# Kernel optimization log

Measured on AMD Instinct MI355X. Metric: run time of the kernel, lower is better.

Reference implementation:

```python
import jax, jax.numpy as jnp
import numpy as np

B, Q, DIM, HEADS, RPE_H, HGRID, WGRID, STRIDE = 2, 900, 256, 8, 512, 64, 64, 16
KV = HGRID * WGRID


def setup_inputs() -> dict:
    key = jax.random.key(0)
    ks = jax.random.split(key, 16)
    s = 0.02
    return {
        "hidden_states": jax.random.normal(ks[0], (B, Q, DIM), jnp.float32),
        "reference_points": jax.random.uniform(ks[1], (B, Q, 1, 4), jnp.float32),
        "key_value_states": jax.random.normal(ks[2], (B, KV, DIM), jnp.float32),
        "spatial_shapes": jnp.array([[HGRID, WGRID]], dtype=jnp.int64),
        "attention_mask": jax.random.randint(ks[3], (B, KV), 0, 2, jnp.int32),
        "mlp1_w1": jax.random.normal(ks[4], (RPE_H, 2), jnp.float32) * s,
        "mlp1_b1": jnp.zeros((RPE_H,), jnp.float32),
        "mlp1_w2": jax.random.normal(ks[5], (HEADS, RPE_H), jnp.float32) * s,
        "mlp2_w1": jax.random.normal(ks[6], (RPE_H, 2), jnp.float32) * s,
        "mlp2_b1": jnp.zeros((RPE_H,), jnp.float32),
        "mlp2_w2": jax.random.normal(ks[7], (HEADS, RPE_H), jnp.float32) * s,
        "q_w": jax.random.normal(ks[8], (DIM, DIM), jnp.float32) * s,
        "q_b": jnp.zeros((DIM,), jnp.float32),
        "k_w": jax.random.normal(ks[9], (DIM, DIM), jnp.float32) * s,
        "k_b": jnp.zeros((DIM,), jnp.float32),
        "v_w": jax.random.normal(ks[10], (DIM, DIM), jnp.float32) * s,
        "v_b": jnp.zeros((DIM,), jnp.float32),
        "o_w": jax.random.normal(ks[11], (DIM, DIM), jnp.float32) * s,
        "o_b": jnp.zeros((DIM,), jnp.float32),
    }


def _attn(hidden_states, reference_points, key_value_states, h, w, attention_mask,
          mlp1_w1, mlp1_b1, mlp1_w2, mlp2_w1, mlp2_b1, mlp2_w2,
          q_w, q_b, k_w, k_b, v_w, v_b, o_w, o_b):
    b, q_len, dim = hidden_states.shape
    nh = mlp1_w2.shape[0]
    hd = dim // nh
    scale = hd ** -0.5
    stride = STRIDE

    # boxes cxcywh -> x1y1x2y2, scaled to absolute pixel coords (reparam=False)
    c, sz = reference_points[..., :2], reference_points[..., 2:]
    ref = jnp.concatenate([c - sz / 2, c + sz / 2], axis=-1)  # (B,Q,1,4)
    mult = jnp.array([w * stride, h * stride, w * stride, h * stride], dtype=ref.dtype)
    ref = ref * mult

    pos_x = (jnp.arange(w, dtype=jnp.float32) + 0.5) * stride
    pos_y = (jnp.arange(h, dtype=jnp.float32) + 0.5) * stride
    dx = ref[..., 0::2] - pos_x[None, None, :, None]  # (B,Q,W,2)
    dy = ref[..., 1::2] - pos_y[None, None, :, None]  # (B,Q,H,2)

    # small MLPs: 2 -> rpe_hidden -> num_heads
    rpe_x = jax.nn.relu(dx @ mlp1_w1.T + mlp1_b1) @ mlp1_w2.T  # (B,Q,W,nh)
    rpe_y = jax.nn.relu(dy @ mlp2_w1.T + mlp2_b1) @ mlp2_w2.T  # (B,Q,H,nh)
    rpe = rpe_x[:, :, None, :, :] + rpe_y[:, :, :, None, :]    # (B,Q,H,W,nh)
    rpe = rpe.reshape(b, q_len, h * w, nh).transpose(0, 3, 1, 2)  # (B,nh,Q,K)

    queries = (hidden_states @ q_w.T + q_b).reshape(b, q_len, nh, hd).transpose(0, 2, 1, 3) * scale
    kv_len = key_value_states.shape[1]
    keys = (key_value_states @ k_w.T + k_b).reshape(b, kv_len, nh, hd).transpose(0, 2, 1, 3)
    values = (key_value_states @ v_w.T + v_b).reshape(b, kv_len, nh, hd).transpose(0, 2, 1, 3)

    scores = jnp.einsum('bhqd,bhkd->bhqk', queries, keys) + rpe
    scores = scores + attention_mask.astype(scores.dtype)[:, None, None] * (-100.0)
    probs = jax.nn.softmax(scores, axis=-1)
    ctx = jnp.einsum('bhqk,bhkd->bhqd', probs, values)
    ctx = ctx.transpose(0, 2, 1, 3).reshape(b, q_len, dim)
    return ctx @ o_w.T + o_b


def reference(hidden_states, reference_points, key_value_states, spatial_shapes, attention_mask,
              mlp1_w1, mlp1_b1, mlp1_w2, mlp2_w1, mlp2_b1, mlp2_w2,
              q_w, q_b, k_w, k_b, v_w, v_b, o_w, o_b):
    h = int(spatial_shapes[0, 0])
    w = int(spatial_shapes[0, 1])
    return _attn(hidden_states, reference_points, key_value_states, h, w, attention_mask,
                 mlp1_w1, mlp1_b1, mlp1_w2, mlp2_w1, mlp2_b1, mlp2_w2,
                 q_w, q_b, k_w, k_b, v_w, v_b, o_w, o_b)
```

## Files before the change

### kernel.cpp

```cpp
#include <hip/hip_runtime.h>
#include <math.h>

#define NB    2
#define NQ    900
#define NQP   960
#define NKV   4096
#define DIMM  256
#define NHEAD 8
#define HD    32
#define RPEH  512
#define GRID  64
#define SPLIT 4
#define KVSEG 1024
#define NT    16

typedef short short8 __attribute__((ext_vector_type(8)));
typedef float f32x4 __attribute__((ext_vector_type(4)));
typedef unsigned uint2v __attribute__((ext_vector_type(2)));
typedef unsigned short u16;
typedef unsigned short u16x4 __attribute__((ext_vector_type(4)));

__device__ inline u16 f2bf(float f) {
    unsigned u = __builtin_bit_cast(unsigned, f);
    u += 0x7fff + ((u >> 16) & 1);
    return (u16)(u >> 16);
}
__device__ inline unsigned packbf2(float a, float b) {
    unsigned ua = __builtin_bit_cast(unsigned, a);
    ua += 0x7fff + ((ua >> 16) & 1);
    unsigned ub = __builtin_bit_cast(unsigned, b);
    ub += 0x7fff + ((ub >> 16) & 1);
    return (ua >> 16) | (ub & 0xffff0000u);
}

#define HS4  115200
#define KV4  524288
#define W4   16384
__global__ __launch_bounds__(256) void conv_bf16(
    const float* __restrict__ hs, const float* __restrict__ kv,
    const float* __restrict__ qw, const float* __restrict__ kw,
    const float* __restrict__ vw,
    u16* __restrict__ hsbf, u16* __restrict__ kvbf,
    u16* __restrict__ qwbf, u16* __restrict__ kwbf, u16* __restrict__ vwbf)
{
    const int total = HS4 + KV4 + 3 * W4;
    for (int g = blockIdx.x * 256 + threadIdx.x; g < total; g += gridDim.x * 256) {
        const float* s; u16* d; int off;
        if (g < HS4)                       { s = hs; d = hsbf; off = g; }
        else if (g < HS4 + KV4)            { s = kv; d = kvbf; off = g - HS4; }
        else if (g < HS4 + KV4 + W4)       { s = qw; d = qwbf; off = g - HS4 - KV4; }
        else if (g < HS4 + KV4 + 2 * W4)   { s = kw; d = kwbf; off = g - HS4 - KV4 - W4; }
        else                               { s = vw; d = vwbf; off = g - HS4 - KV4 - 2 * W4; }
        f32x4 v = *(const f32x4*)(s + (size_t)off * 4);
        *(u16x4*)(d + (size_t)off * 4) =
            (u16x4){f2bf(v[0]), f2bf(v[1]), f2bf(v[2]), f2bf(v[3])};
    }
}

__global__ __launch_bounds__(256) void proj_mfma(
    const u16* __restrict__ A,
    const u16* __restrict__ W0, const float* __restrict__ B0,
    const u16* __restrict__ W1, const float* __restrict__ B1,
    u16* __restrict__ outRow, u16* __restrict__ outVt,
    int M, float scale)
{
    __shared__ u16 Abuf[2][4096];
    __shared__ u16 Bbuf[2][4096];

    const u16* W = W0; const float* bias = B0; bool vt = false;
    if (blockIdx.z == 1) { W = W1; bias = B1; vt = true; }

    const int t    = threadIdx.x;
    const int lane = t & 63;
    const int w    = t >> 6;
    const int wm   = w >> 1, wn = w & 1;
    const int m0   = blockIdx.x * 128;
    const int n0   = blockIdx.y * 128;

    const int r0 = t >> 2, c0 = t & 3;
    const int r1 = r0 + 64;
    const int s0 = r0 * 4 + (c0 ^ (r0 & 3));
    const int s1 = r1 * 4 + (c0 ^ (r1 & 3));
    const u16* Arow0 = A + (size_t)(m0 + r0) * DIMM + c0 * 8;
    const u16* Arow1 = A + (size_t)(m0 + r1) * DIMM + c0 * 8;
    const u16* Wrow0 = W + (size_t)(n0 + r0) * DIMM + c0 * 8;
    const u16* Wrow1 = W + (size_t)(n0 + r1) * DIMM + c0 * 8;

    const int fr = lane & 15, fkc = lane >> 4;
    int aslot[4], bslot[4];
    #pragma unroll
    for (int f = 0; f < 4; ++f) {
        int ar = wm * 64 + f * 16 + fr;
        int br = wn * 64 + f * 16 + fr;
        aslot[f] = ar * 4 + (fkc ^ (ar & 3));
        bslot[f] = br * 4 + (fkc ^ (br & 3));
    }
    float bv[4];
    #pragma unroll
    for (int f = 0; f < 4; ++f) bv[f] = bias[n0 + wn * 64 + f * 16 + fr];

    f32x4 acc[4][4] = {};

    {
        short8 a0 = *(const short8*)(Arow0);
        short8 a1 = *(const short8*)(Arow1);
        short8 b0 = *(const short8*)(Wrow0);
        short8 b1 = *(const short8*)(Wrow1);
        *(short8*)&Abuf[0][s0 * 8] = a0;
        *(short8*)&Abuf[0][s1 * 8] = a1;
        *(short8*)&Bbuf[0][s0 * 8] = b0;
        *(short8*)&Bbuf[0][s1 * 8] = b1;
    }
    __syncthreads();

    int cur = 0;
    for (int kt = 0; kt < 8; ++kt) {
        short8 na0, na1, nb0, nb1;
        if (kt < 7) {
            int ko = (kt + 1) * 32;
            na0 = *(const short8*)(Arow0 + ko);
            na1 = *(const short8*)(Arow1 + ko);
            nb0 = *(const short8*)(Wrow0 + ko);
            nb1 = *(const short8*)(Wrow1 + ko);
        }
        short8 af[4], bf[4];
        #pragma unroll
        for (int f = 0; f < 4; ++f) {
            af[f] = *(const short8*)&Abuf[cur][aslot[f] * 8];
            bf[f] = *(const short8*)&Bbuf[cur][bslot[f] * 8];
        }
        #pragma unroll
        for (int i = 0; i < 4; ++i)
            #pragma unroll
            for (int j = 0; j < 4; ++j)
                acc[i][j] = __builtin_amdgcn_mfma_f32_16x16x32_bf16(af[i], bf[j], acc[i][j], 0, 0, 0);
        if (kt < 7) {
            *(short8*)&Abuf[cur ^ 1][s0 * 8] = na0;
            *(short8*)&Abuf[cur ^ 1][s1 * 8] = na1;
            *(short8*)&Bbuf[cur ^ 1][s0 * 8] = nb0;
            *(short8*)&Bbuf[cur ^ 1][s1 * 8] = nb1;
        }
        __syncthreads();
        cur ^= 1;
    }

    #pragma unroll
    for (int i = 0; i < 4; ++i) {
        int mbase = m0 + wm * 64 + i * 16 + 4 * fkc;
        #pragma unroll
        for (int j = 0; j < 4; ++j) {
            int n = n0 + wn * 64 + j * 16 + fr;
            #pragma unroll
            for (int r = 0; r < 4; ++r) {
                int gm = mbase + r;
                if (gm < M) {
                    float v = (acc[i][j][r] + bv[j]) * scale;
                    if (!vt) {
                        outRow[(size_t)gm * DIMM + n] = f2bf(v);
                    } else {
                        int bb = gm >> 12, kvi = gm & 4095;
                        int hh = n >> 5, dd = n & 31;
                        outVt[(size_t)((bb * NHEAD + hh) * HD + dd) * NKV + kvi] = f2bf(v);
                    }
                }
            }
        }
    }
}

__global__ __launch_bounds__(256) void rpe_kernel(
    const float* __restrict__ ref_pts,
    const float* __restrict__ w1x, const float* __restrict__ b1x,
    const float* __restrict__ w2x,
    const float* __restrict__ w1y, const float* __restrict__ b1y,
    const float* __restrict__ w2y,
    float* __restrict__ rpex, float* __restrict__ rpey)
{
    __shared__ f32x4 wpk[RPEH];
    __shared__ float w2t[RPEH][NHEAD];

    const int t = threadIdx.x;
    const int m = blockIdx.x & 1;
    const int bq0 = (blockIdx.x >> 1) * 4;

    const float* w1 = m ? w1y : w1x;
    const float* b1 = m ? b1y : b1x;
    const float* w2 = m ? w2y : w2x;
    for (int r = t; r < RPEH; r += 256) {
        float a = w1[r * 2], b = w1[r * 2 + 1];
        wpk[r] = (f32x4){a, b, b1[r], a + b};
    }
    for (int i = t; i < RPEH * NHEAD; i += 256) {
        int h = i >> 9, r = i & 511;
        w2t[r][h] = w2[h * RPEH + r];
    }
    __syncthreads();

    const int lane = t & 63;
    const int w    = t >> 6;
    const int bq   = bq0 + w;
    const float p  = (lane + 0.5f) * 16.f;

    const float* q = ref_pts + (size_t)bq * 4;
    const float c = m ? q[1] : q[0];
    const float s = m ? q[3] : q[2];
    const float lo = (c - s * 0.5f) * 1024.f;
    const float hi = (c + s * 0.5f) * 1024.f;

    float acc[8] = {};
    #pragma unroll 4
    for (int r = 0; r < RPEH; ++r) {
        f32x4 W  = wpk[r];
        f32x4 u0 = *(const f32x4*)&w2t[r][0];
        f32x4 u1 = *(const f32x4*)&w2t[r][4];
        float al  = W[0] * lo + W[1] * hi + W[2];
        float hid = fmaxf(al - W[3] * p, 0.f);
        acc[0] += u0[0] * hid;
        acc[1] += u0[1] * hid;
        acc[2] += u0[2] * hid;
        acc[3] += u0[3] * hid;
        acc[4] += u1[0] * hid;
        acc[5] += u1[1] * hid;
        acc[6] += u1[2] * hid;
        acc[7] += u1[3] * hid;
    }

    float* outp = m ? rpey : rpex;
    size_t base = (size_t)bq * (NHEAD * GRID) + lane;
    #pragma unroll
    for (int h = 0; h < 8; ++h) outp[base + h * GRID] = acc[h];
}

__global__ __launch_bounds__(256) void attn_mfma(
    const u16* __restrict__ Qbf, const u16* __restrict__ Kbf,
    const u16* __restrict__ Vt,
    const float* __restrict__ RX, const float* __restrict__ RY,
    const int* __restrict__ mask,
    float* __restrict__ pctx, float2* __restrict__ pml)
{
    __shared__ short8 kbuf[2][4][64];
    __shared__ short8 vbuf[2][4][64];
    __shared__ unsigned pbuf[4][2][64][4];
    __shared__ float ry_s[16][68];
    __shared__ float mbuf[2][64];

    const int tid  = threadIdx.x;
    const int lane = tid & 63;
    const int w    = tid >> 6;
    const int q15  = lane & 15;
    const int g    = lane >> 4;
    const int qt = blockIdx.x, h = blockIdx.y;
    const int b  = blockIdx.z >> 2;
    const int sp = blockIdx.z & 3;
    const int q0 = qt * 64;
    const int wq = w * 16 + q15;
    const int gq = q0 + wq;
    const bool qok = gq < NQ;
    const int kv0g = sp * KVSEG;

    float rxr[16];
    {
        const float* rxrow = RX + (size_t)(b * NQ + (qok ? gq : 0)) * (NHEAD * GRID) + h * GRID;
        #pragma unroll
        for (int kt = 0; kt < 4; ++kt)
            #pragma unroll
            for (int r = 0; r < 4; ++r)
                rxr[kt * 4 + r] = qok ? rxrow[16 * kt + 4 * g + r] : 0.f;
    }
    for (int idx = tid; idx < 16 * 64; idx += 256) {
        int y = idx & 15, q = idx >> 4;
        int gq2 = q0 + q;
        ry_s[y][q] = (gq2 < NQ)
            ? RY[(size_t)(b * NQ + gq2) * (NHEAD * GRID) + h * GRID + sp * 16 + y] : 0.f;
    }

    short8 qf = *(const short8*)(Qbf + ((size_t)(b * NQ + gq)) * DIMM + h * HD + 8 * g);

    const int sr = tid >> 2, sc = tid & 3;
    const int vd = tid >> 3, vc = tid & 7;
    const size_t kbase = ((size_t)(b * NKV + kv0g + sr)) * DIMM + h * HD + 8 * sc;
    const size_t vbase = ((size_t)((b * NHEAD + h) * HD + vd)) * NKV + kv0g + 8 * vc;

    kbuf[0][sr >> 4][(sr & 15) + 16 * sc] = *(const short8*)(Kbf + kbase);
    vbuf[0][(vc >> 2) * 2 + (vd >> 4)][16 * (vc & 3) + (vd & 15)] = *(const short8*)(Vt + vbase);
    if (tid < 64) mbuf[0][tid] = -100.f * (float)mask[b * NKV + kv0g + tid];
    __syncthreads();

    f32x4 cacc0 = {0.f, 0.f, 0.f, 0.f};
    f32x4 cacc1 = {0.f, 0.f, 0.f, 0.f};
    float m_run = -1e30f, l_run = 0.f;
    int cur = 0;

    for (int t = 0; t < NT; ++t) {
        short8 rk = {}, rv = {};
        float rm = 0.f;
        if (t < NT - 1) {
            size_t kvn = (size_t)(t + 1) * 64;
            rk = *(const short8*)(Kbf + kbase + kvn * DIMM);
            rv = *(const short8*)(Vt + vbase + kvn);
            if (tid < 64) rm = -100.f * (float)mask[b * NKV + kv0g + kvn + tid];
        }

        f32x4 zero = {0.f, 0.f, 0.f, 0.f};
        f32x4 s[4];
        __builtin_amdgcn_s_setprio(1);
        #pragma unroll
        for (int kt = 0; kt < 4; ++kt)
            s[kt] = __builtin_amdgcn_mfma_f32_16x16x32_bf16(kbuf[cur][kt][lane], qf, zero, 0, 0, 0);
        __builtin_amdgcn_s_setprio(0);

        float ryb = ry_s[t][wq];
        #pragma unroll
        for (int kt = 0; kt < 4; ++kt) {
            #pragma unroll
            for (int r = 0; r < 4; ++r)
                s[kt][r] += rxr[kt * 4 + r] + ryb + mbuf[cur][16 * kt + 4 * g + r];
        }

        float mloc = s[0][0];
        #pragma unroll
        for (int kt = 0; kt < 4; ++kt)
            #pragma unroll
            for (int r = 0; r < 4; ++r) mloc = fmaxf(mloc, s[kt][r]);
        mloc = fmaxf(mloc, __shfl_xor(mloc, 16));
        mloc = fmaxf(mloc, __shfl_xor(mloc, 32));
        float mnew = fmaxf(m_run, mloc);
        float fsc  = __expf(m_run - mnew);
        float psum = 0.f;
        #pragma unroll
        for (int kt = 0; kt < 4; ++kt)
            #pragma unroll
            for (int r = 0; r < 4; ++r) {
                float pv = __expf(s[kt][r] - mnew);
                s[kt][r] = pv;
                psum += pv;
            }
        psum += __shfl_xor(psum, 16);
        psum += __shfl_xor(psum, 32);
        l_run = l_run * fsc + psum;
        m_run = mnew;
        cacc0 *= fsc;
        cacc1 *= fsc;

        #pragma unroll
        for (int kt = 0; kt < 4; ++kt) {
            unsigned d0 = packbf2(s[kt][0], s[kt][1]);
            unsigned d1 = packbf2(s[kt][2], s[kt][3]);
            int lt = 16 * ((2 * kt + (g >> 1)) & 3) + q15;
            uint2v* dst = (uint2v*)&pbuf[w][kt >> 1][lt][2 * (g & 1)];
            *dst = (uint2v){d0, d1};
        }

        __builtin_amdgcn_s_setprio(1);
        #pragma unroll
        for (int sk = 0; sk < 2; ++sk) {
            short8 pf = *(const short8*)&pbuf[w][sk][lane][0];
            cacc0 = __builtin_amdgcn_mfma_f32_16x16x32_bf16(vbuf[cur][sk * 2 + 0][lane], pf, cacc0, 0, 0, 0);
            cacc1 = __builtin_amdgcn_mfma_f32_16x16x32_bf16(vbuf[cur][sk * 2 + 1][lane], pf, cacc1, 0, 0, 0);
        }
        __builtin_amdgcn_s_setprio(0);

        if (t < NT - 1) {
            kbuf[cur ^ 1][sr >> 4][(sr & 15) + 16 * sc] = rk;
            vbuf[cur ^ 1][(vc >> 2) * 2 + (vd >> 4)][16 * (vc & 3) + (vd & 15)] = rv;
            if (tid < 64) mbuf[cur ^ 1][tid] = rm;
        }
        __syncthreads();
        cur ^= 1;
    }

    size_t prow = (size_t)(sp * NB + b) * NQP + gq;
    float* pc = pctx + prow * DIMM + h * HD;
    #pragma unroll
    for (int r = 0; r < 4; ++r) {
        pc[4 * g + r]      = cacc0[r];
        pc[16 + 4 * g + r] = cacc1[r];
    }
    if (g == 0) {
        float2 v; v.x = m_run; v.y = l_run;
        pml[prow * NHEAD + h] = v;
    }
}

__global__ __launch_bounds__(256) void attn_reduce(
    const float* __restrict__ pctx, const float2* __restrict__ pml,
    float* __restrict__ CTX)
{
    const int bq = blockIdx.x;
    const int b = bq / NQ, q = bq - b * NQ;
    const int c = threadIdx.x;
    const int h = c >> 5;

    float m[SPLIT], l[SPLIT];
    #pragma unroll
    for (int sp = 0; sp < SPLIT; ++sp) {
        float2 v = pml[((size_t)(sp * NB + b) * NQP + q) * NHEAD + h];
        m[sp] = v.x; l[sp] = v.y;
    }
    float ms = fmaxf(fmaxf(m[0], m[1]), fmaxf(m[2], m[3]));
    float L = 0.f, acc = 0.f;
    #pragma unroll
    for (int sp = 0; sp < SPLIT; ++sp) {
        float wgt = __expf(m[sp] - ms);
        L   += wgt * l[sp];
        acc += wgt * pctx[((size_t)(sp * NB + b) * NQP + q) * DIMM + c];
    }
    CTX[(size_t)bq * DIMM + c] = acc / L;
}

__global__ __launch_bounds__(256) void gemm_bias_f32(
    const float* __restrict__ A, const float* __restrict__ W,
    const float* __restrict__ bias, float* __restrict__ C,
    int M, int N, int K)
{
    __shared__ float As[32][33];
    __shared__ float Ws[32][33];
    const int t  = threadIdx.x;
    const int tr = t >> 4;
    const int tc = t & 15;
    const int brow = blockIdx.y * 32;
    const int bcol = blockIdx.x * 32;
    float acc00 = 0.f, acc01 = 0.f, acc10 = 0.f, acc11 = 0.f;

    for (int kt = 0; kt < K; kt += 32) {
        #pragma unroll
        for (int i = 0; i < 4; ++i) {
            int idx = t + i * 256;
            int r = idx >> 5, c = idx & 31;
            int gr = brow + r;
            As[r][c] = (gr < M) ? A[(size_t)gr * K + kt + c] : 0.f;
            Ws[r][c] = W[(size_t)(bcol + r) * K + kt + c];
        }
        __syncthreads();
        #pragma unroll 8
        for (int k = 0; k < 32; ++k) {
            float a0 = As[tr * 2][k], a1 = As[tr * 2 + 1][k];
            float w0 = Ws[tc * 2][k], w1 = Ws[tc * 2 + 1][k];
            acc00 += a0 * w0; acc01 += a0 * w1;
            acc10 += a1 * w0; acc11 += a1 * w1;
        }
        __syncthreads();
    }
    int gc0 = bcol + tc * 2, gc1 = gc0 + 1;
    int gr0 = brow + tr * 2, gr1 = gr0 + 1;
    if (gr0 < M) {
        C[(size_t)gr0 * N + gc0] = acc00 + bias[gc0];
        C[(size_t)gr0 * N + gc1] = acc01 + bias[gc1];
    }
    if (gr1 < M) {
        C[(size_t)gr1 * N + gc0] = acc10 + bias[gc0];
        C[(size_t)gr1 * N + gc1] = acc11 + bias[gc1];
    }
}

extern "C" void kernel_launch(void* const* d_in, const int* in_sizes, int n_in,
                              void* d_out, int out_size, void* d_ws, size_t ws_size,
                              hipStream_t stream)
{
    const float* hs   = (const float*)d_in[0];
    const float* rp   = (const float*)d_in[1];
    const float* kv   = (const float*)d_in[2];
    const int*   msk  = (const int*)d_in[4];
    const float* m1w1 = (const float*)d_in[5];
    const float* m1b1 = (const float*)d_in[6];
    const float* m1w2 = (const float*)d_in[7];
    const float* m2w1 = (const float*)d_in[8];
    const float* m2b1 = (const float*)d_in[9];
    const float* m2w2 = (const float*)d_in[10];
    const float* q_w  = (const float*)d_in[11];
    const float* q_b  = (const float*)d_in[12];
    const float* k_w  = (const float*)d_in[13];
    const float* k_b  = (const float*)d_in[14];
    const float* v_w  = (const float*)d_in[15];
    const float* v_b  = (const float*)d_in[16];
    const float* o_w  = (const float*)d_in[17];
    const float* o_b  = (const float*)d_in[18];
    float* out = (float*)d_out;

    char* p = (char*)d_ws;
    float* RX   = (float*)p; p += (size_t)NB * NQ * NHEAD * GRID * 4;
    float* RY   = (float*)p; p += (size_t)NB * NQ * NHEAD * GRID * 4;
    float* CTX  = (float*)p; p += (size_t)NB * NQ * DIMM * 4;
    u16*   Qbf  = (u16*)p;   p += (size_t)1920 * DIMM * 2;
    u16*   Kbf  = (u16*)p;   p += (size_t)NB * NKV * DIMM * 2;
    u16*   Vt   = (u16*)p;   p += (size_t)NB * NHEAD * HD * NKV * 2;

    char* u = p;
    u16* hsbf = (u16*)u;
    u16* kvbf = hsbf + (size_t)1920 * DIMM;
    u16* qwbf = kvbf + (size_t)NB * NKV * DIMM;
    u16* kwbf = qwbf + (size_t)DIMM * DIMM;
    u16* vwbf = kwbf + (size_t)DIMM * DIMM;
    float*  pctx = (float*)u;
    float2* pml  = (float2*)(pctx + (size_t)SPLIT * NB * NQP * DIMM);

    const float scale = 0.17677669529663687f;

    conv_bf16<<<1024, 256, 0, stream>>>(hs, kv, q_w, k_w, v_w,
                                        hsbf, kvbf, qwbf, kwbf, vwbf);

    proj_mfma<<<dim3(15, 2, 1), 256, 0, stream>>>(
        hsbf, qwbf, q_b, nullptr, nullptr, Qbf, nullptr, NB * NQ, scale);

    proj_mfma<<<dim3(64, 2, 2), 256, 0, stream>>>(
        kvbf, kwbf, k_b, vwbf, v_b, Kbf, Vt, NB * NKV, 1.f);

    rpe_kernel<<<900, 256, 0, stream>>>(rp, m1w1, m1b1, m1w2,
                                        m2w1, m2b1, m2w2, RX, RY);

    attn_mfma<<<dim3((NQ + 63) / 64, NHEAD, NB * SPLIT), 256, 0, stream>>>(
        Qbf, Kbf, Vt, RX, RY, msk, pctx, pml);

    attn_reduce<<<NB * NQ, 256, 0, stream>>>(pctx, pml, CTX);

    gemm_bias_f32<<<dim3(DIMM / 32, (NB * NQ + 31) / 32), 256, 0, stream>>>(
        CTX, o_w, o_b, out, NB * NQ, DIMM, DIMM);
}
```

Baseline: 151.3 us.

## Prepack RPE MLP weights once and split hidden dim across two waves

Adds a small kernel that packs both RPE MLPs' first-layer weights, bias, and second-layer weights into a contiguous 12-float-per-row global buffer. Each RPE block no longer rebuilds shared-memory weight tables, which removes the redundant per-block staging and the barrier. The RPE kernel now uses 3600 blocks of 128 threads. Each of the two waves covers half the 512 hidden units and reads weights directly from global memory (wave-uniform, cached), and the halves are combined through shared memory. The cost is an extra launch and global/scalar loads in the inner loop instead of LDS reads.

Result: slower. 265.3 us (+75.3%).

```diff
diff --git a/kernel.cpp b/kernel.cpp
--- a/kernel.cpp
+++ b/kernel.cpp
@@ -55,6 +55,30 @@
         *(u16x4*)(d + (size_t)off * 4) =
             (u16x4){f2bf(v[0]), f2bf(v[1]), f2bf(v[2]), f2bf(v[3])};
     }
+}
+
+__global__ __launch_bounds__(256) void rpe_pack(
+    const float* __restrict__ w1x, const float* __restrict__ b1x,
+    const float* __restrict__ w2x,
+    const float* __restrict__ w1y, const float* __restrict__ b1y,
+    const float* __restrict__ w2y,
+    float* __restrict__ wpkg)
+{
+    int i = blockIdx.x * 256 + threadIdx.x;
+    if (i >= 2 * RPEH * 12) return;
+    int m = i / (RPEH * 12);
+    int rem = i - m * RPEH * 12;
+    int r = rem / 12, j = rem - r * 12;
+    const float* w1 = m ? w1y : w1x;
+    const float* b1 = m ? b1y : b1x;
+    const float* w2 = m ? w2y : w2x;
+    float v;
+    if (j == 0)      v = w1[r * 2];
+    else if (j == 1) v = w1[r * 2 + 1];
+    else if (j == 2) v = b1[r];
+    else if (j == 3) v = w1[r * 2] + w1[r * 2 + 1];
+    else             v = w2[(j - 4) * RPEH + r];
+    wpkg[i] = v;
 }
 
 __global__ __launch_bounds__(256) void proj_mfma(
@@ -168,37 +192,18 @@
     }
 }
 
-__global__ __launch_bounds__(256) void rpe_kernel(
+__global__ __launch_bounds__(128) void rpe_kernel(
     const float* __restrict__ ref_pts,
-    const float* __restrict__ w1x, const float* __restrict__ b1x,
-    const float* __restrict__ w2x,
-    const float* __restrict__ w1y, const float* __restrict__ b1y,
-    const float* __restrict__ w2y,
+    const float* __restrict__ wpkg,
     float* __restrict__ rpex, float* __restrict__ rpey)
 {
-    __shared__ f32x4 wpk[RPEH];
-    __shared__ float w2t[RPEH][NHEAD];
-
-    const int t = threadIdx.x;
-    const int m = blockIdx.x & 1;
-    const int bq0 = (blockIdx.x >> 1) * 4;
-
-    const float* w1 = m ? w1y : w1x;
-    const float* b1 = m ? b1y : b1x;
-    const float* w2 = m ? w2y : w2x;
-    for (int r = t; r < RPEH; r += 256) {
-        float a = w1[r * 2], b = w1[r * 2 + 1];
-        wpk[r] = (f32x4){a, b, b1[r], a + b};
-    }
-    for (int i = t; i < RPEH * NHEAD; i += 256) {
-        int h = i >> 9, r = i & 511;
-        w2t[r][h] = w2[h * RPEH + r];
-    }
-    __syncthreads();
-
+    __shared__ float red[8][64];
+    const int t    = threadIdx.x;
     const int lane = t & 63;
     const int w    = t >> 6;
-    const int bq   = bq0 + w;
+    const int task = blockIdx.x;
+    const int m    = task & 1;
+    const int bq   = task >> 1;
     const float p  = (lane + 0.5f) * 16.f;
 
     const float* q = ref_pts + (size_t)bq * 4;
@@ -207,28 +212,40 @@
     const float lo = (c - s * 0.5f) * 1024.f;
     const float hi = (c + s * 0.5f) * 1024.f;
 
-    float acc[8] = {};
-    #pragma unroll 4
-    for (int r = 0; r < RPEH; ++r) {
-        f32x4 W  = wpk[r];
-        f32x4 u0 = *(const f32x4*)&w2t[r][0];
-        f32x4 u1 = *(const f32x4*)&w2t[r][4];
-        float al  = W[0] * lo + W[1] * hi + W[2];
-        float hid = fmaxf(al - W[3] * p, 0.f);
-        acc[0] += u0[0] * hid;
-        acc[1] += u0[1] * hid;
-        acc[2] += u0[2] * hid;
-        acc[3] += u0[3] * hid;
-        acc[4] += u1[0] * hid;
-        acc[5] += u1[1] * hid;
-        acc[6] += u1[2] * hid;
-        acc[7] += u1[3] * hid;
-    }
-
-    float* outp = m ? rpey : rpex;
-    size_t base = (size_t)bq * (NHEAD * GRID) + lane;
-    #pragma unroll
-    for (int h = 0; h < 8; ++h) outp[base + h * GRID] = acc[h];
+    const float* wp = wpkg + ((size_t)m * RPEH + w * 256) * 12;
+
+    float2 acc[4] = {};
+    #pragma unroll 2
+    for (int r = 0; r < 256; ++r) {
+        const float* wr = wp + r * 12;
+        float a = wr[0], b = wr[1], bias = wr[2], ab = wr[3];
+        float al  = a * lo + b * hi + bias;
+        float hid = fmaxf(al - ab * p, 0.f);
+        #pragma unroll
+        for (int j = 0; j < 4; ++j) {
+            float2 w2 = *(const float2*)(wr + 4 + 2 * j);
+            acc[j].x += w2.x * hid;
+            acc[j].y += w2.y * hid;
+        }
+    }
+
+    if (w == 1) {
+        #pragma unroll
+        for (int j = 0; j < 4; ++j) {
+            red[2 * j][lane]     = acc[j].x;
+            red[2 * j + 1][lane] = acc[j].y;
+        }
+    }
+    __syncthreads();
+    if (w == 0) {
+        float* outp = m ? rpey : rpex;
+        size_t base = (size_t)bq * (NHEAD * GRID) + lane;
+        #pragma unroll
+        for (int j = 0; j < 4; ++j) {
+            outp[base + (2 * j) * GRID]     = acc[j].x + red[2 * j][lane];
+            outp[base + (2 * j + 1) * GRID] = acc[j].y + red[2 * j + 1][lane];
+        }
+    }
 }
 
 __global__ __launch_bounds__(256) void attn_mfma(
@@ -484,6 +501,7 @@
     u16*   Qbf  = (u16*)p;   p += (size_t)1920 * DIMM * 2;
     u16*   Kbf  = (u16*)p;   p += (size_t)NB * NKV * DIMM * 2;
     u16*   Vt   = (u16*)p;   p += (size_t)NB * NHEAD * HD * NKV * 2;
+    float* WPKG = (float*)p; p += (size_t)2 * RPEH * 12 * 4;
 
     char* u = p;
     u16* hsbf = (u16*)u;
@@ -496,6 +514,8 @@
 
     const float scale = 0.17677669529663687f;
 
+    rpe_pack<<<48, 256, 0, stream>>>(m1w1, m1b1, m1w2, m2w1, m2b1, m2w2, WPKG);
+
     conv_bf16<<<1024, 256, 0, stream>>>(hs, kv, q_w, k_w, v_w,
                                         hsbf, kvbf, qwbf, kwbf, vwbf);
 
@@ -505,8 +525,7 @@
     proj_mfma<<<dim3(64, 2, 2), 256, 0, stream>>>(
         kvbf, kwbf, k_b, vwbf, v_b, Kbf, Vt, NB * NKV, 1.f);
 
-    rpe_kernel<<<900, 256, 0, stream>>>(rp, m1w1, m1b1, m1w2,
-                                        m2w1, m2b1, m2w2, RX, RY);
+    rpe_kernel<<<3600, 128, 0, stream>>>(rp, WPKG, RX, RY);
 
     attn_mfma<<<dim3((NQ + 63) / 64, NHEAD, NB * SPLIT), 256, 0, stream>>>(
         Qbf, Kbf, Vt, RX, RY, msk, pctx, pml);
```

## Split KV across waves in attention and share RPE rows across queries

Applied to the files above, without the earlier changes.

The attention kernel now gives each block 16 queries and splits its KV segment across four waves. Each wave loads its own K/V tiles straight into private LDS slots, with no block-wide barriers in the loop, and the waves' softmax partials are merged through shared memory at the end. The RPE kernel now has each wave process a quarter of the hidden units for four queries and reduces across waves, which reuses the weight loads. This trades more blocks and redundant Q and RX loads for fewer barriers and less serialization. There is a risk of lower K/V reuse across queries, since each K tile is now loaded for only 16 queries.

New measurement: 189.7 us. +25.4%, slower.

```diff
diff --git a/kernel.cpp b/kernel.cpp
--- a/kernel.cpp
+++ b/kernel.cpp
@@ -11,8 +11,6 @@
 #define RPEH  512
 #define GRID  64
 #define SPLIT 4
-#define KVSEG 1024
-#define NT    16
 
 typedef short short8 __attribute__((ext_vector_type(8)));
 typedef float f32x4 __attribute__((ext_vector_type(4)));
@@ -178,9 +176,10 @@
 {
     __shared__ f32x4 wpk[RPEH];
     __shared__ float w2t[RPEH][NHEAD];
-
-    const int t = threadIdx.x;
-    const int m = blockIdx.x & 1;
+    __shared__ float2 red[3][4][4][64];
+
+    const int t   = threadIdx.x;
+    const int m   = blockIdx.x & 1;
     const int bq0 = (blockIdx.x >> 1) * 4;
 
     const float* w1 = m ? w1y : w1x;
@@ -197,38 +196,64 @@
     __syncthreads();
 
     const int lane = t & 63;
-    const int w    = t >> 6;
-    const int bq   = bq0 + w;
+    const int wv   = t >> 6;
     const float p  = (lane + 0.5f) * 16.f;
 
-    const float* q = ref_pts + (size_t)bq * 4;
-    const float c = m ? q[1] : q[0];
-    const float s = m ? q[3] : q[2];
-    const float lo = (c - s * 0.5f) * 1024.f;
-    const float hi = (c + s * 0.5f) * 1024.f;
-
-    float acc[8] = {};
+    float lo[4], hi[4];
+    #pragma unroll
+    for (int j = 0; j < 4; ++j) {
+        const float* q = ref_pts + (size_t)(bq0 + j) * 4;
+        float c = m ? q[1] : q[0];
+        float s = m ? q[3] : q[2];
+        lo[j] = (c - s * 0.5f) * 1024.f;
+        hi[j] = (c + s * 0.5f) * 1024.f;
+    }
+
+    float2 acc[4][4] = {};
+    const int r0 = wv * 128;
     #pragma unroll 4
-    for (int r = 0; r < RPEH; ++r) {
+    for (int rr = 0; rr < 128; ++rr) {
+        int r = r0 + rr;
         f32x4 W  = wpk[r];
         f32x4 u0 = *(const f32x4*)&w2t[r][0];
         f32x4 u1 = *(const f32x4*)&w2t[r][4];
-        float al  = W[0] * lo + W[1] * hi + W[2];
-        float hid = fmaxf(al - W[3] * p, 0.f);
-        acc[0] += u0[0] * hid;
-        acc[1] += u0[1] * hid;
-        acc[2] += u0[2] * hid;
-        acc[3] += u0[3] * hid;
-        acc[4] += u1[0] * hid;
-        acc[5] += u1[1] * hid;
-        acc[6] += u1[2] * hid;
-        acc[7] += u1[3] * hid;
-    }
-
-    float* outp = m ? rpey : rpex;
-    size_t base = (size_t)bq * (NHEAD * GRID) + lane;
-    #pragma unroll
-    for (int h = 0; h < 8; ++h) outp[base + h * GRID] = acc[h];
+        float bp = W[3] * p;
+        #pragma unroll
+        for (int tk = 0; tk < 4; ++tk) {
+            float al  = W[0] * lo[tk] + W[1] * hi[tk] + W[2];
+            float hid = fmaxf(al - bp, 0.f);
+            acc[tk][0].x += u0[0] * hid;  acc[tk][0].y += u0[1] * hid;
+            acc[tk][1].x += u0[2] * hid;  acc[tk][1].y += u0[3] * hid;
+            acc[tk][2].x += u1[0] * hid;  acc[tk][2].y += u1[1] * hid;
+            acc[tk][3].x += u1[2] * hid;  acc[tk][3].y += u1[3] * hid;
+        }
+    }
+
+    if (wv > 0) {
+        #pragma unroll
+        for (int tk = 0; tk < 4; ++tk)
+            #pragma unroll
+            for (int j = 0; j < 4; ++j)
+                red[wv - 1][tk][j][lane] = acc[tk][j];
+    }
+    __syncthreads();
+    if (wv == 0) {
+        float* outp = m ? rpey : rpex;
+        #pragma unroll
+        for (int tk = 0; tk < 4; ++tk) {
+            size_t base = (size_t)(bq0 + tk) * (NHEAD * GRID) + lane;
+            #pragma unroll
+            for (int j = 0; j < 4; ++j) {
+                float2 s0 = red[0][tk][j][lane];
+                float2 s1 = red[1][tk][j][lane];
+                float2 s2 = red[2][tk][j][lane];
+                float sx = acc[tk][j].x + s0.x + s1.x + s2.x;
+                float sy = acc[tk][j].y + s0.y + s1.y + s2.y;
+                outp[base + (2 * j) * GRID]     = sx;
+                outp[base + (2 * j + 1) * GRID] = sy;
+            }
+        }
+    }
 }
 
 __global__ __launch_bounds__(256) void attn_mfma(
@@ -238,11 +263,11 @@
     const int* __restrict__ mask,
     float* __restrict__ pctx, float2* __restrict__ pml)
 {
-    __shared__ short8 kbuf[2][4][64];
-    __shared__ short8 vbuf[2][4][64];
+    __shared__ short8 kbuf[4][4][64];
+    __shared__ short8 vbuf[4][4][64];
     __shared__ unsigned pbuf[4][2][64][4];
-    __shared__ float ry_s[16][68];
-    __shared__ float mbuf[2][64];
+    __shared__ float mbuf[4][64];
+    __shared__ float comb[3][64][11];
 
     const int tid  = threadIdx.x;
     const int lane = tid & 63;
@@ -252,53 +277,63 @@
     const int qt = blockIdx.x, h = blockIdx.y;
     const int b  = blockIdx.z >> 2;
     const int sp = blockIdx.z & 3;
-    const int q0 = qt * 64;
-    const int wq = w * 16 + q15;
-    const int gq = q0 + wq;
+    const int q0 = qt * 16;
+    const int gq = q0 + q15;
     const bool qok = gq < NQ;
-    const int kv0g = sp * KVSEG;
-
-    float rxr[16];
+    const int kv0g = sp * 1024 + w * 256;
+
+    float rxr[16], ryr[4];
     {
-        const float* rxrow = RX + (size_t)(b * NQ + (qok ? gq : 0)) * (NHEAD * GRID) + h * GRID;
+        const float* base = RX + (size_t)(b * NQ + (qok ? gq : 0)) * (NHEAD * GRID) + h * GRID;
         #pragma unroll
         for (int kt = 0; kt < 4; ++kt)
             #pragma unroll
             for (int r = 0; r < 4; ++r)
-                rxr[kt * 4 + r] = qok ? rxrow[16 * kt + 4 * g + r] : 0.f;
-    }
-    for (int idx = tid; idx < 16 * 64; idx += 256) {
-        int y = idx & 15, q = idx >> 4;
-        int gq2 = q0 + q;
-        ry_s[y][q] = (gq2 < NQ)
-            ? RY[(size_t)(b * NQ + gq2) * (NHEAD * GRID) + h * GRID + sp * 16 + y] : 0.f;
+                rxr[kt * 4 + r] = qok ? base[16 * kt + 4 * g + r] : 0.f;
+        const float* ybase = RY + (size_t)(b * NQ + (qok ? gq : 0)) * (NHEAD * GRID) + h * GRID;
+        #pragma unroll
+        for (int t = 0; t < 4; ++t)
+            ryr[t] = qok ? ybase[sp * 16 + w * 4 + t] : 0.f;
     }
 
     short8 qf = *(const short8*)(Qbf + ((size_t)(b * NQ + gq)) * DIMM + h * HD + 8 * g);
 
-    const int sr = tid >> 2, sc = tid & 3;
-    const int vd = tid >> 3, vc = tid & 7;
-    const size_t kbase = ((size_t)(b * NKV + kv0g + sr)) * DIMM + h * HD + 8 * sc;
-    const size_t vbase = ((size_t)((b * NHEAD + h) * HD + vd)) * NKV + kv0g + 8 * vc;
-
-    kbuf[0][sr >> 4][(sr & 15) + 16 * sc] = *(const short8*)(Kbf + kbase);
-    vbuf[0][(vc >> 2) * 2 + (vd >> 4)][16 * (vc & 3) + (vd & 15)] = *(const short8*)(Vt + vbase);
-    if (tid < 64) mbuf[0][tid] = -100.f * (float)mask[b * NKV + kv0g + tid];
-    __syncthreads();
+    {
+        short8 rk[4], rv[4];
+        #pragma unroll
+        for (int kt = 0; kt < 4; ++kt)
+            rk[kt] = *(const short8*)(Kbf + ((size_t)(b * NKV + kv0g + 16 * kt + q15)) * DIMM + h * HD + 8 * g);
+        #pragma unroll
+        for (int j = 0; j < 4; ++j) {
+            int sk = j >> 1, dt = j & 1;
+            rv[j] = *(const short8*)(Vt + ((size_t)((b * NHEAD + h) * HD + 16 * dt + q15)) * NKV + kv0g + 32 * sk + 8 * g);
+        }
+        float rm = -100.f * (float)mask[b * NKV + kv0g + lane];
+        #pragma unroll
+        for (int kt = 0; kt < 4; ++kt) kbuf[w][kt][lane] = rk[kt];
+        #pragma unroll
+        for (int j = 0; j < 4; ++j) vbuf[w][j][lane] = rv[j];
+        mbuf[w][lane] = rm;
+    }
 
     f32x4 cacc0 = {0.f, 0.f, 0.f, 0.f};
     f32x4 cacc1 = {0.f, 0.f, 0.f, 0.f};
     float m_run = -1e30f, l_run = 0.f;
-    int cur = 0;
-
-    for (int t = 0; t < NT; ++t) {
-        short8 rk = {}, rv = {};
-        float rm = 0.f;
-        if (t < NT - 1) {
-            size_t kvn = (size_t)(t + 1) * 64;
-            rk = *(const short8*)(Kbf + kbase + kvn * DIMM);
-            rv = *(const short8*)(Vt + vbase + kvn);
-            if (tid < 64) rm = -100.f * (float)mask[b * NKV + kv0g + kvn + tid];
+
+    for (int t = 0; t < 4; ++t) {
+        short8 nk[4] = {}, nv[4] = {};
+        float nm = 0.f;
+        if (t < 3) {
+            int kvn = kv0g + (t + 1) * 64;
+            #pragma unroll
+            for (int kt = 0; kt < 4; ++kt)
+                nk[kt] = *(const short8*)(Kbf + ((size_t)(b * NKV + kvn + 16 * kt + q15)) * DIMM + h * HD + 8 * g);
+            #pragma unroll
+            for (int j = 0; j < 4; ++j) {
+                int sk = j >> 1, dt = j & 1;
+                nv[j] = *(const short8*)(Vt + ((size_t)((b * NHEAD + h) * HD + 16 * dt + q15)) * NKV + kvn + 32 * sk + 8 * g);
+            }
+            nm = -100.f * (float)mask[b * NKV + kvn + lane];
         }
 
         f32x4 zero = {0.f, 0.f, 0.f, 0.f};
@@ -306,15 +341,15 @@
         __builtin_amdgcn_s_setprio(1);
         #pragma unroll
         for (int kt = 0; kt < 4; ++kt)
-            s[kt] = __builtin_amdgcn_mfma_f32_16x16x32_bf16(kbuf[cur][kt][lane], qf, zero, 0, 0, 0);
+            s[kt] = __builtin_amdgcn_mfma_f32_16x16x32_bf16(kbuf[w][kt][lane], qf, zero, 0, 0, 0);
         __builtin_amdgcn_s_setprio(0);
 
-        float ryb = ry_s[t][wq];
+        float ryb = ryr[t];
         #pragma unroll
         for (int kt = 0; kt < 4; ++kt) {
             #pragma unroll
             for (int r = 0; r < 4; ++r)
-                s[kt][r] += rxr[kt * 4 + r] + ryb + mbuf[cur][16 * kt + 4 * g + r];
+                s[kt][r] += rxr[kt * 4 + r] + ryb + mbuf[w][16 * kt + 4 * g + r];
         }
 
         float mloc = s[0][0];
@@ -355,30 +390,54 @@
         #pragma unroll
         for (int sk = 0; sk < 2; ++sk) {
             short8 pf = *(const short8*)&pbuf[w][sk][lane][0];
-            cacc0 = __builtin_amdgcn_mfma_f32_16x16x32_bf16(vbuf[cur][sk * 2 + 0][lane], pf, cacc0, 0, 0, 0);
-            cacc1 = __builtin_amdgcn_mfma_f32_16x16x32_bf16(vbuf[cur][sk * 2 + 1][lane], pf, cacc1, 0, 0, 0);
+            cacc0 = __builtin_amdgcn_mfma_f32_16x16x32_bf16(vbuf[w][sk * 2 + 0][lane], pf, cacc0, 0, 0, 0);
+            cacc1 = __builtin_amdgcn_mfma_f32_16x16x32_bf16(vbuf[w][sk * 2 + 1][lane], pf, cacc1, 0, 0, 0);
         }
         __builtin_amdgcn_s_setprio(0);
 
-        if (t < NT - 1) {
-            kbuf[cur ^ 1][sr >> 4][(sr & 15) + 16 * sc] = rk;
-            vbuf[cur ^ 1][(vc >> 2) * 2 + (vd >> 4)][16 * (vc & 3) + (vd & 15)] = rv;
-            if (tid < 64) mbuf[cur ^ 1][tid] = rm;
-        }
-        __syncthreads();
-        cur ^= 1;
-    }
-
-    size_t prow = (size_t)(sp * NB + b) * NQP + gq;
-    float* pc = pctx + prow * DIMM + h * HD;
-    #pragma unroll
-    for (int r = 0; r < 4; ++r) {
-        pc[4 * g + r]      = cacc0[r];
-        pc[16 + 4 * g + r] = cacc1[r];
-    }
-    if (g == 0) {
-        float2 v; v.x = m_run; v.y = l_run;
-        pml[prow * NHEAD + h] = v;
+        if (t < 3) {
+            #pragma unroll
+            for (int kt = 0; kt < 4; ++kt) kbuf[w][kt][lane] = nk[kt];
+            #pragma unroll
+            for (int j = 0; j < 4; ++j) vbuf[w][j][lane] = nv[j];
+            mbuf[w][lane] = nm;
+        }
+    }
+
+    if (w > 0) {
+        float* c = &comb[w - 1][lane][0];
+        c[0] = m_run; c[1] = l_run;
+        #pragma unroll
+        for (int r = 0; r < 4; ++r) { c[2 + r] = cacc0[r]; c[6 + r] = cacc1[r]; }
+    }
+    __syncthreads();
+    if (w == 0) {
+        float M = m_run;
+        #pragma unroll
+        for (int j = 0; j < 3; ++j) M = fmaxf(M, comb[j][lane][0]);
+        float ws = __expf(m_run - M);
+        float L  = ws * l_run;
+        f32x4 o0 = cacc0 * ws;
+        f32x4 o1 = cacc1 * ws;
+        #pragma unroll
+        for (int j = 0; j < 3; ++j) {
+            const float* c = &comb[j][lane][0];
+            float wj = __expf(c[0] - M);
+            L += wj * c[1];
+            #pragma unroll
+            for (int r = 0; r < 4; ++r) { o0[r] += wj * c[2 + r]; o1[r] += wj * c[6 + r]; }
+        }
+        size_t prow = (size_t)(sp * NB + b) * NQP + gq;
+        float* pc = pctx + prow * DIMM + h * HD;
+        #pragma unroll
+        for (int r = 0; r < 4; ++r) {
+            pc[4 * g + r]      = o0[r];
+            pc[16 + 4 * g + r] = o1[r];
+        }
+        if (g == 0) {
+            float2 v; v.x = M; v.y = L;
+            pml[prow * NHEAD + h] = v;
+        }
     }
 }
 
@@ -508,7 +567,7 @@
     rpe_kernel<<<900, 256, 0, stream>>>(rp, m1w1, m1b1, m1w2,
                                         m2w1, m2b1, m2w2, RX, RY);
 
-    attn_mfma<<<dim3((NQ + 63) / 64, NHEAD, NB * SPLIT), 256, 0, stream>>>(
+    attn_mfma<<<dim3((NQ + 15) / 16, NHEAD, NB * SPLIT), 256, 0, stream>>>(
         Qbf, Kbf, Vt, RX, RY, msk, pctx, pml);
 
     attn_reduce<<<NB * NQ, 256, 0, stream>>>(pctx, pml, CTX);
```
